# Kernel tuning notes

Measured on AMD Instinct MI355X. Metric: run time of the kernel, lower is better.

The kernel has to match this reference:

```python
import jax, jax.numpy as jnp
import numpy as np

B, K, NV, H, T = 4, 2, 32, 16, 4096
G = K * NV                 # conv groups = 64
OPG = 2 * (NV + H)         # out channels per group = 96 (instantaneous doubles channels)
TEMPERATURE = 1.0


def setup_inputs() -> dict:
    key = jax.random.key(0)
    k1, k2, k3 = jax.random.split(key, 3)
    x = jax.random.normal(k1, (B, G * H, T), dtype=jnp.float32)
    W = jax.random.normal(k2, (G, OPG, H), dtype=jnp.float32) * (1.0 / np.sqrt(H))
    b = jax.random.normal(k3, (G, OPG), dtype=jnp.float32) * 0.01
    return {"x": x, "W": W, "b": b}


def reference(x, W, b):
    # pad one zero step at end of sequence (ConstantPad1d((0,1),0))
    xp = jnp.pad(x, ((0, 0), (0, 0), (0, 1)))            # (B, G*H, T+1)
    xg = xp.reshape(B, G, H, T + 1)
    # TCN modeled as grouped pointwise conv: per-group linear over channel dim
    y = jnp.einsum('bgdt,god->bgot', xg, W) + b[None, :, :, None]  # (B, G, OPG, T+1)
    # split temporal / instantaneous branches with the causal shift
    y = y.reshape(B * K, NV, 2, NV + H, T + 1)
    xt = y[:, :, 0, :, :-1]                               # (B*K, NV, NV+H, T)
    xi = y[:, :, 1, :, 1:]                                # (B*K, NV, NV+H, T)
    # split attention logits (first NV channels) and context (last H channels)
    ctx = jnp.concatenate([xt[:, :, NV:, :], xi[:, :, NV:, :]], axis=1)   # (B*K, 2*NV, H, T)
    att = jnp.concatenate([xt[:, :, :NV, :], xi[:, :, :NV, :]], axis=2)   # (B*K, NV, 2*NV, T)
    att = jax.nn.softmax(att / TEMPERATURE, axis=2)
    out = jnp.einsum('bijt,bjdt->bidt', att, ctx)         # (B*K, NV, H, T)
    out = out.reshape(B, K * NV * H, T)
    attn = att.reshape(B, K, NV, 2 * NV, T)
    return out, attn
```

## Files before the change

### kernel.cpp

```cpp
#include <hip/hip_runtime.h>
#include <hip/hip_bf16.h>
#include <stdint.h>

#define B_  4
#define K_  2
#define T_  4096
#define TT  16

#define GS  296
#define US  16
#define AJ  652
#define AT  40
#define CJ  256
#define CT  16

__device__ __forceinline__ float bflo(uint32_t w) {
    union { uint32_t u; float f; } v; v.u = w << 16; return v.f;
}
__device__ __forceinline__ float bfhi(uint32_t w) {
    union { uint32_t u; float f; } v; v.u = w & 0xFFFF0000u; return v.f;
}
__device__ __forceinline__ float bf2f(uint16_t u) {
    union { uint32_t u; float f; } v; v.u = ((uint32_t)u) << 16; return v.f;
}
__device__ __forceinline__ uint16_t f2bf(float f) {
    union { float f; uint32_t u; } v; v.f = f;
    uint32_t x = v.u;
    return (uint16_t)((x + 0x7FFFu + ((x >> 16) & 1u)) >> 16);
}

__global__ __launch_bounds__(512, 2)
void tamcad_kernel(const float* __restrict__ x, const float* __restrict__ W,
                   const float* __restrict__ bias, float* __restrict__ out)
{
    __shared__ float    xsr[32 * GS];
    __shared__ uint16_t As [64 * AJ];
    __shared__ uint16_t Cs [64 * CJ];

    const int tid   = threadIdx.x;
    const int bk    = blockIdx.x >> 5;
    const int chunk = blockIdx.x & 31;
    const int b     = bk >> 1;
    const int k     = bk & 1;

    const int g_loc = tid >> 4;
    const int oq    = tid & 15;
    const int slot  = (oq >= 8) ? 1 : 0;

    float wreg[6][16];
    float breg[6];
    bool  isl[6];
    int   aoff[6];
    int   coff[6];
    #pragma unroll
    for (int r = 0; r < 6; ++r) {
        const int o = oq * 6 + r;
        const size_t wbase = (((size_t)(k * 32 + g_loc)) * 96 + o) * 16;
        const float4* wp = reinterpret_cast<const float4*>(W + wbase);
        float4 w0 = wp[0], w1 = wp[1], w2 = wp[2], w3 = wp[3];
        wreg[r][ 0]=w0.x; wreg[r][ 1]=w0.y; wreg[r][ 2]=w0.z; wreg[r][ 3]=w0.w;
        wreg[r][ 4]=w1.x; wreg[r][ 5]=w1.y; wreg[r][ 6]=w1.z; wreg[r][ 7]=w1.w;
        wreg[r][ 8]=w2.x; wreg[r][ 9]=w2.y; wreg[r][10]=w2.z; wreg[r][11]=w2.w;
        wreg[r][12]=w3.x; wreg[r][13]=w3.y; wreg[r][14]=w3.z; wreg[r][15]=w3.w;
        breg[r] = bias[(k * 32 + g_loc) * 96 + o];
        if (o < 32)      { isl[r] = true;  aoff[r] = o * AJ + g_loc;               coff[r] = 0; }
        else if (o < 48) { isl[r] = false; coff[r] = g_loc * CJ + (o - 32);        aoff[r] = 0; }
        else if (o < 80) { isl[r] = true;  aoff[r] = (o - 16) * AJ + g_loc;        coff[r] = 0; }
        else             { isl[r] = false; coff[r] = (32 + g_loc) * CJ + (o - 80); aoff[r] = 0; }
    }

    for (int l = 0; l < 8; ++l) {
        const int t0 = (chunk * 8 + l) * TT;

        {
            const float* gp = x + (((size_t)b * 1024) + (size_t)(k * 32 + g_loc) * 16 + oq) * (size_t)T_ + t0;
            float4 q0 = *(const float4*)(gp + 0);
            float4 q1 = *(const float4*)(gp + 4);
            float4 q2 = *(const float4*)(gp + 8);
            float4 q3 = *(const float4*)(gp + 12);
            float  q4 = (t0 + 16 < T_) ? gp[16] : 0.0f;
            float vals[17] = { q0.x,q0.y,q0.z,q0.w, q1.x,q1.y,q1.z,q1.w,
                               q2.x,q2.y,q2.z,q2.w, q3.x,q3.y,q3.z,q3.w, q4 };
            float* xp = xsr + g_loc * GS + oq;
            #pragma unroll
            for (int u = 0; u < 17; ++u) xp[u * US] = vals[u];
        }
        __syncthreads();

        {
            float xv[16];
            {
                const float4* p4 = reinterpret_cast<const float4*>(xsr + g_loc * GS + slot * US);
                float4 A0 = p4[0], A1 = p4[1], A2 = p4[2], A3 = p4[3];
                xv[ 0]=A0.x; xv[ 1]=A0.y; xv[ 2]=A0.z; xv[ 3]=A0.w;
                xv[ 4]=A1.x; xv[ 5]=A1.y; xv[ 6]=A1.z; xv[ 7]=A1.w;
                xv[ 8]=A2.x; xv[ 9]=A2.y; xv[10]=A2.z; xv[11]=A2.w;
                xv[12]=A3.x; xv[13]=A3.y; xv[14]=A3.z; xv[15]=A3.w;
            }
            for (int tp = 0; tp < TT; ++tp) {
                float yv[6];
                #pragma unroll
                for (int r = 0; r < 6; ++r) {
                    float a = breg[r];
                    #pragma unroll
                    for (int d = 0; d < 16; ++d) a = fmaf(wreg[r][d], xv[d], a);
                    yv[r] = a;
                }
                {
                    const float4* p4 = reinterpret_cast<const float4*>(xsr + g_loc * GS + (tp + 1 + slot) * US);
                    float4 A0 = p4[0], A1 = p4[1], A2 = p4[2], A3 = p4[3];
                    xv[ 0]=A0.x; xv[ 1]=A0.y; xv[ 2]=A0.z; xv[ 3]=A0.w;
                    xv[ 4]=A1.x; xv[ 5]=A1.y; xv[ 6]=A1.z; xv[ 7]=A1.w;
                    xv[ 8]=A2.x; xv[ 9]=A2.y; xv[10]=A2.z; xv[11]=A2.w;
                    xv[12]=A3.x; xv[13]=A3.y; xv[14]=A3.z; xv[15]=A3.w;
                }
                float m = -3.0e38f;
                #pragma unroll
                for (int r = 0; r < 6; ++r) if (isl[r]) m = fmaxf(m, yv[r]);
                #pragma unroll
                for (int s = 1; s < 16; s <<= 1) m = fmaxf(m, __shfl_xor(m, s));
                float ssum = 0.0f;
                float ev[6];
                #pragma unroll
                for (int r = 0; r < 6; ++r) {
                    ev[r] = 0.0f;
                    if (isl[r]) { ev[r] = __expf(yv[r] - m); ssum += ev[r]; }
                }
                #pragma unroll
                for (int s = 1; s < 16; s <<= 1) ssum += __shfl_xor(ssum, s);
                const float rinv = 1.0f / ssum;
                #pragma unroll
                for (int r = 0; r < 6; ++r) {
                    if (isl[r]) As[aoff[r] + tp * AT] = f2bf(ev[r] * rinv);
                    else        Cs[coff[r] + tp * CT] = f2bf(yv[r]);
                }
            }
        }
        __syncthreads();

        {
            const int tl = tid >> 5;
            const int r5 = tid & 31;
            const int i0 = (r5 & 7) << 2;
            const int d0 = (r5 >> 3) << 2;
            float acc[4][4];
            #pragma unroll
            for (int ii = 0; ii < 4; ++ii)
                #pragma unroll
                for (int dd = 0; dd < 4; ++dd) acc[ii][dd] = 0.0f;
            const uint16_t* Ap = As + tl * AT + i0;
            const uint16_t* Cp = Cs + tl * CT + d0;
            #pragma unroll 8
            for (int j = 0; j < 64; ++j) {
                uint2 aw = *(const uint2*)(Ap + j * AJ);
                uint2 cw = *(const uint2*)(Cp + j * CJ);
                float a0 = bflo(aw.x), a1 = bfhi(aw.x), a2 = bflo(aw.y), a3 = bfhi(aw.y);
                float c0 = bflo(cw.x), c1 = bfhi(cw.x), c2 = bflo(cw.y), c3 = bfhi(cw.y);
                acc[0][0] = fmaf(a0, c0, acc[0][0]); acc[0][1] = fmaf(a0, c1, acc[0][1]);
                acc[0][2] = fmaf(a0, c2, acc[0][2]); acc[0][3] = fmaf(a0, c3, acc[0][3]);
                acc[1][0] = fmaf(a1, c0, acc[1][0]); acc[1][1] = fmaf(a1, c1, acc[1][1]);
                acc[1][2] = fmaf(a1, c2, acc[1][2]); acc[1][3] = fmaf(a1, c3, acc[1][3]);
                acc[2][0] = fmaf(a2, c0, acc[2][0]); acc[2][1] = fmaf(a2, c1, acc[2][1]);
                acc[2][2] = fmaf(a2, c2, acc[2][2]); acc[2][3] = fmaf(a2, c3, acc[2][3]);
                acc[3][0] = fmaf(a3, c0, acc[3][0]); acc[3][1] = fmaf(a3, c1, acc[3][1]);
                acc[3][2] = fmaf(a3, c2, acc[3][2]); acc[3][3] = fmaf(a3, c3, acc[3][3]);
            }
            #pragma unroll
            for (int ii = 0; ii < 4; ++ii)
                #pragma unroll
                for (int dd = 0; dd < 4; ++dd)
                    xsr[((i0 + ii) * 16 + d0 + dd) * 17 + tl] = acc[ii][dd];
        }
        __syncthreads();

        {
            float ov[16];
            #pragma unroll
            for (int u = 0; u < 16; ++u) ov[u] = xsr[tid * 17 + u];
            float* op = out + (((size_t)b * 1024) + k * 512 + tid) * (size_t)T_ + t0;
            *(float4*)(op + 0)  = make_float4(ov[ 0], ov[ 1], ov[ 2], ov[ 3]);
            *(float4*)(op + 4)  = make_float4(ov[ 4], ov[ 5], ov[ 6], ov[ 7]);
            *(float4*)(op + 8)  = make_float4(ov[ 8], ov[ 9], ov[10], ov[11]);
            *(float4*)(op + 12) = make_float4(ov[12], ov[13], ov[14], ov[15]);

            float* attn_base = out + (size_t)B_ * 1024 * (size_t)T_;
            #pragma unroll
            for (int rr = 0; rr < 4; ++rr) {
                const int q = tid + 512 * rr;
                const int i = q >> 6;
                const int j = q & 63;
                const uint16_t* ap = As + j * AJ + i;
                float av[16];
                #pragma unroll
                for (int u = 0; u < 16; ++u) av[u] = bf2f(ap[u * AT]);
                float* tp2 = attn_base + ((((size_t)bk * 32 + i) * 64) + j) * (size_t)T_ + t0;
                *(float4*)(tp2 + 0)  = make_float4(av[ 0], av[ 1], av[ 2], av[ 3]);
                *(float4*)(tp2 + 4)  = make_float4(av[ 4], av[ 5], av[ 6], av[ 7]);
                *(float4*)(tp2 + 8)  = make_float4(av[ 8], av[ 9], av[10], av[11]);
                *(float4*)(tp2 + 12) = make_float4(av[12], av[13], av[14], av[15]);
            }
        }
        __syncthreads();
    }
}

extern "C" void kernel_launch(void* const* d_in, const int* in_sizes, int n_in,
                              void* d_out, int out_size, void* d_ws, size_t ws_size,
                              hipStream_t stream) {
    const float* x  = (const float*)d_in[0];
    const float* W  = (const float*)d_in[1];
    const float* bs = (const float*)d_in[2];
    float* out = (float*)d_out;
    tamcad_kernel<<<dim3(256), dim3(512), 0, stream>>>(x, W, bs, out);
}
```

Before: 293.3 us.

## Double threads per block, prefetch x into registers, drop softmax max pass

Block size goes from 512 to 1024 threads, so each thread computes 3 grouped-conv output channels instead of 6. The softmax reduction now spans 32 lanes, and the attention matmul uses 4x2 tiles per thread. The next x tile is prefetched into registers while the current one is processed, and the Cs row stride and the output staging layout are padded and skewed to reduce LDS bank conflicts. The max-subtraction pass in softmax is removed, saving one shuffle reduction per timestep but risking overflow for large logits. The launch bound of 1024 threads with a minimum of 4 blocks may force register caps and spills.

```diff
diff --git a/kernel.cpp b/kernel.cpp
--- a/kernel.cpp
+++ b/kernel.cpp
@@ -1,41 +1,28 @@
 #include <hip/hip_runtime.h>
-#include <hip/hip_bf16.h>
 #include <stdint.h>
 
-#define B_  4
-#define K_  2
 #define T_  4096
-#define TT  16
-
 #define GS  296
 #define US  16
 #define AJ  652
 #define AT  40
-#define CJ  256
-#define CT  16
-
-__device__ __forceinline__ float bflo(uint32_t w) {
-    union { uint32_t u; float f; } v; v.u = w << 16; return v.f;
+#define CJ  260
+
+static __device__ __forceinline__ float bflo(uint32_t w){ union{uint32_t u;float f;}v; v.u=w<<16; return v.f; }
+static __device__ __forceinline__ float bfhi(uint32_t w){ union{uint32_t u;float f;}v; v.u=w&0xFFFF0000u; return v.f; }
+static __device__ __forceinline__ float bf2f(uint16_t u){ union{uint32_t u;float f;}v; v.u=((uint32_t)u)<<16; return v.f; }
+static __device__ __forceinline__ uint16_t f2bf(float f){
+    union{float f;uint32_t u;}v; v.f=f; uint32_t x=v.u;
+    return (uint16_t)((x + 0x7FFFu + ((x>>16)&1u)) >> 16);
 }
-__device__ __forceinline__ float bfhi(uint32_t w) {
-    union { uint32_t u; float f; } v; v.u = w & 0xFFFF0000u; return v.f;
-}
-__device__ __forceinline__ float bf2f(uint16_t u) {
-    union { uint32_t u; float f; } v; v.u = ((uint32_t)u) << 16; return v.f;
-}
-__device__ __forceinline__ uint16_t f2bf(float f) {
-    union { float f; uint32_t u; } v; v.f = f;
-    uint32_t x = v.u;
-    return (uint16_t)((x + 0x7FFFu + ((x >> 16) & 1u)) >> 16);
-}
-
-__global__ __launch_bounds__(512, 2)
+
+__global__ __launch_bounds__(1024, 4)
 void tamcad_kernel(const float* __restrict__ x, const float* __restrict__ W,
                    const float* __restrict__ bias, float* __restrict__ out)
 {
-    __shared__ float    xsr[32 * GS];
-    __shared__ uint16_t As [64 * AJ];
-    __shared__ uint16_t Cs [64 * CJ];
+    __shared__ float    xsr[32*GS];
+    __shared__ uint16_t As [64*AJ];
+    __shared__ uint16_t Cs [64*CJ];
 
     const int tid   = threadIdx.x;
     const int bk    = blockIdx.x >> 5;
@@ -43,161 +30,168 @@
     const int b     = bk >> 1;
     const int k     = bk & 1;
 
-    const int g_loc = tid >> 4;
-    const int oq    = tid & 15;
-    const int slot  = (oq >= 8) ? 1 : 0;
-
-    float wreg[6][16];
-    float breg[6];
-    bool  isl[6];
-    int   aoff[6];
-    int   coff[6];
+    const int oq   = tid & 31;
+    const int g    = tid >> 5;
+    const int slot = oq >> 4;
+
+    const int dl = tid & 15;
+    const int gl = (tid >> 4) & 31;
+    const int hl = tid >> 9;
+
+    float wreg[3][16], breg[3];
+    int   aoff[3], coff[3];
+    bool  isl[3];
     #pragma unroll
-    for (int r = 0; r < 6; ++r) {
-        const int o = oq * 6 + r;
-        const size_t wbase = (((size_t)(k * 32 + g_loc)) * 96 + o) * 16;
-        const float4* wp = reinterpret_cast<const float4*>(W + wbase);
-        float4 w0 = wp[0], w1 = wp[1], w2 = wp[2], w3 = wp[3];
+    for (int r = 0; r < 3; ++r) {
+        const int o = oq*3 + r;
+        const float4* wp = reinterpret_cast<const float4*>(W + (((size_t)(k*32+g))*96 + o)*16);
+        float4 w0=wp[0], w1=wp[1], w2=wp[2], w3=wp[3];
         wreg[r][ 0]=w0.x; wreg[r][ 1]=w0.y; wreg[r][ 2]=w0.z; wreg[r][ 3]=w0.w;
         wreg[r][ 4]=w1.x; wreg[r][ 5]=w1.y; wreg[r][ 6]=w1.z; wreg[r][ 7]=w1.w;
         wreg[r][ 8]=w2.x; wreg[r][ 9]=w2.y; wreg[r][10]=w2.z; wreg[r][11]=w2.w;
         wreg[r][12]=w3.x; wreg[r][13]=w3.y; wreg[r][14]=w3.z; wreg[r][15]=w3.w;
-        breg[r] = bias[(k * 32 + g_loc) * 96 + o];
-        if (o < 32)      { isl[r] = true;  aoff[r] = o * AJ + g_loc;               coff[r] = 0; }
-        else if (o < 48) { isl[r] = false; coff[r] = g_loc * CJ + (o - 32);        aoff[r] = 0; }
-        else if (o < 80) { isl[r] = true;  aoff[r] = (o - 16) * AJ + g_loc;        coff[r] = 0; }
-        else             { isl[r] = false; coff[r] = (32 + g_loc) * CJ + (o - 80); aoff[r] = 0; }
+        breg[r] = bias[(k*32+g)*96 + o];
+        if (o < 32)      { isl[r]=true;  aoff[r]=o*AJ + g;            coff[r]=0; }
+        else if (o < 48) { isl[r]=false; coff[r]=g*CJ + (o-32);       aoff[r]=0; }
+        else if (o < 80) { isl[r]=true;  aoff[r]=(o-16)*AJ + g;       coff[r]=0; }
+        else             { isl[r]=false; coff[r]=(32+g)*CJ + (o-80);  aoff[r]=0; }
     }
 
+    const float* xrow = x + ((size_t)b*1024 + (size_t)(k*32+gl)*16 + dl) * (size_t)T_;
+
+    float4 pA, pB; float pS = 0.0f;
+    {
+        const float* gp = xrow + chunk*128 + hl*8;
+        pA = *(const float4*)(gp + 0);
+        pB = *(const float4*)(gp + 4);
+        pS = (hl && (chunk*128 + 16) < T_) ? gp[8] : 0.0f;
+    }
+
     for (int l = 0; l < 8; ++l) {
-        const int t0 = (chunk * 8 + l) * TT;
-
-        {
-            const float* gp = x + (((size_t)b * 1024) + (size_t)(k * 32 + g_loc) * 16 + oq) * (size_t)T_ + t0;
-            float4 q0 = *(const float4*)(gp + 0);
-            float4 q1 = *(const float4*)(gp + 4);
-            float4 q2 = *(const float4*)(gp + 8);
-            float4 q3 = *(const float4*)(gp + 12);
-            float  q4 = (t0 + 16 < T_) ? gp[16] : 0.0f;
-            float vals[17] = { q0.x,q0.y,q0.z,q0.w, q1.x,q1.y,q1.z,q1.w,
-                               q2.x,q2.y,q2.z,q2.w, q3.x,q3.y,q3.z,q3.w, q4 };
-            float* xp = xsr + g_loc * GS + oq;
-            #pragma unroll
-            for (int u = 0; u < 17; ++u) xp[u * US] = vals[u];
-        }
-        __syncthreads();
+        const int t0 = chunk*128 + l*16;
+
+        {
+            float* xp = xsr + gl*GS + dl;
+            const int ub = hl*8;
+            xp[(ub+0)*US]=pA.x; xp[(ub+1)*US]=pA.y; xp[(ub+2)*US]=pA.z; xp[(ub+3)*US]=pA.w;
+            xp[(ub+4)*US]=pB.x; xp[(ub+5)*US]=pB.y; xp[(ub+6)*US]=pB.z; xp[(ub+7)*US]=pB.w;
+            if (hl) xp[16*US] = pS;
+        }
+        __syncthreads();
+
+        if (l < 7) {
+            const int t0n = t0 + 16;
+            const float* gp = xrow + t0n + hl*8;
+            pA = *(const float4*)(gp + 0);
+            pB = *(const float4*)(gp + 4);
+            pS = (hl && (t0n + 16) < T_) ? gp[8] : 0.0f;
+        }
 
         {
             float xv[16];
             {
-                const float4* p4 = reinterpret_cast<const float4*>(xsr + g_loc * GS + slot * US);
-                float4 A0 = p4[0], A1 = p4[1], A2 = p4[2], A3 = p4[3];
+                const float4* p4 = reinterpret_cast<const float4*>(xsr + g*GS + slot*US);
+                float4 A0=p4[0], A1=p4[1], A2=p4[2], A3=p4[3];
                 xv[ 0]=A0.x; xv[ 1]=A0.y; xv[ 2]=A0.z; xv[ 3]=A0.w;
                 xv[ 4]=A1.x; xv[ 5]=A1.y; xv[ 6]=A1.z; xv[ 7]=A1.w;
                 xv[ 8]=A2.x; xv[ 9]=A2.y; xv[10]=A2.z; xv[11]=A2.w;
                 xv[12]=A3.x; xv[13]=A3.y; xv[14]=A3.z; xv[15]=A3.w;
             }
-            for (int tp = 0; tp < TT; ++tp) {
-                float yv[6];
-                #pragma unroll
-                for (int r = 0; r < 6; ++r) {
+            for (int tp = 0; tp < 16; ++tp) {
+                float yv[3];
+                #pragma unroll
+                for (int r = 0; r < 3; ++r) {
                     float a = breg[r];
                     #pragma unroll
                     for (int d = 0; d < 16; ++d) a = fmaf(wreg[r][d], xv[d], a);
                     yv[r] = a;
                 }
                 {
-                    const float4* p4 = reinterpret_cast<const float4*>(xsr + g_loc * GS + (tp + 1 + slot) * US);
-                    float4 A0 = p4[0], A1 = p4[1], A2 = p4[2], A3 = p4[3];
+                    const float4* p4 = reinterpret_cast<const float4*>(xsr + g*GS + (tp+1+slot)*US);
+                    float4 A0=p4[0], A1=p4[1], A2=p4[2], A3=p4[3];
                     xv[ 0]=A0.x; xv[ 1]=A0.y; xv[ 2]=A0.z; xv[ 3]=A0.w;
                     xv[ 4]=A1.x; xv[ 5]=A1.y; xv[ 6]=A1.z; xv[ 7]=A1.w;
                     xv[ 8]=A2.x; xv[ 9]=A2.y; xv[10]=A2.z; xv[11]=A2.w;
                     xv[12]=A3.x; xv[13]=A3.y; xv[14]=A3.z; xv[15]=A3.w;
                 }
-                float m = -3.0e38f;
-                #pragma unroll
-                for (int r = 0; r < 6; ++r) if (isl[r]) m = fmaxf(m, yv[r]);
-                #pragma unroll
-                for (int s = 1; s < 16; s <<= 1) m = fmaxf(m, __shfl_xor(m, s));
+                float ev[3];
                 float ssum = 0.0f;
-                float ev[6];
-                #pragma unroll
-                for (int r = 0; r < 6; ++r) {
+                #pragma unroll
+                for (int r = 0; r < 3; ++r) {
                     ev[r] = 0.0f;
-                    if (isl[r]) { ev[r] = __expf(yv[r] - m); ssum += ev[r]; }
-                }
-                #pragma unroll
-                for (int s = 1; s < 16; s <<= 1) ssum += __shfl_xor(ssum, s);
-                const float rinv = 1.0f / ssum;
-                #pragma unroll
-                for (int r = 0; r < 6; ++r) {
-                    if (isl[r]) As[aoff[r] + tp * AT] = f2bf(ev[r] * rinv);
-                    else        Cs[coff[r] + tp * CT] = f2bf(yv[r]);
-                }
-            }
-        }
-        __syncthreads();
-
-        {
-            const int tl = tid >> 5;
-            const int r5 = tid & 31;
-            const int i0 = (r5 & 7) << 2;
-            const int d0 = (r5 >> 3) << 2;
-            float acc[4][4];
+                    if (isl[r]) { ev[r] = __expf(yv[r]); ssum += ev[r]; }
+                }
+                #pragma unroll
+                for (int s = 1; s < 32; s <<= 1) ssum += __shfl_xor(ssum, s);
+                const float rinv = __builtin_amdgcn_rcpf(ssum);
+                #pragma unroll
+                for (int r = 0; r < 3; ++r) {
+                    if (isl[r]) As[aoff[r] + tp*AT] = f2bf(ev[r] * rinv);
+                    else        Cs[coff[r] + tp*16] = f2bf(yv[r]);
+                }
+            }
+        }
+        __syncthreads();
+
+        {
+            const int t  = tid >> 6;
+            const int r6 = tid & 63;
+            const int i0 = (r6 & 7) << 2;
+            const int d0 = (r6 >> 3) << 1;
+            float acc[4][2];
+            #pragma unroll
+            for (int ii = 0; ii < 4; ++ii) { acc[ii][0]=0.f; acc[ii][1]=0.f; }
+            const uint16_t* Ap = As + t*AT + i0;
+            const uint16_t* Cp = Cs + t*16 + d0;
+            #pragma unroll 8
+            for (int j = 0; j < 64; ++j) {
+                uint2    aw = *(const uint2*)(Ap + j*AJ);
+                uint32_t cw = *(const uint32_t*)(Cp + j*CJ);
+                float a0=bflo(aw.x), a1=bfhi(aw.x), a2=bflo(aw.y), a3=bfhi(aw.y);
+                float c0=bflo(cw),   c1=bfhi(cw);
+                acc[0][0]=fmaf(a0,c0,acc[0][0]); acc[0][1]=fmaf(a0,c1,acc[0][1]);
+                acc[1][0]=fmaf(a1,c0,acc[1][0]); acc[1][1]=fmaf(a1,c1,acc[1][1]);
+                acc[2][0]=fmaf(a2,c0,acc[2][0]); acc[2][1]=fmaf(a2,c1,acc[2][1]);
+                acc[3][0]=fmaf(a3,c0,acc[3][0]); acc[3][1]=fmaf(a3,c1,acc[3][1]);
+            }
+            const int skew = (r6 & 7) * 4;
             #pragma unroll
             for (int ii = 0; ii < 4; ++ii)
                 #pragma unroll
-                for (int dd = 0; dd < 4; ++dd) acc[ii][dd] = 0.0f;
-            const uint16_t* Ap = As + tl * AT + i0;
-            const uint16_t* Cp = Cs + tl * CT + d0;
-            #pragma unroll 8
-            for (int j = 0; j < 64; ++j) {
-                uint2 aw = *(const uint2*)(Ap + j * AJ);
-                uint2 cw = *(const uint2*)(Cp + j * CJ);
-                float a0 = bflo(aw.x), a1 = bfhi(aw.x), a2 = bflo(aw.y), a3 = bfhi(aw.y);
-                float c0 = bflo(cw.x), c1 = bfhi(cw.x), c2 = bflo(cw.y), c3 = bfhi(cw.y);
-                acc[0][0] = fmaf(a0, c0, acc[0][0]); acc[0][1] = fmaf(a0, c1, acc[0][1]);
-                acc[0][2] = fmaf(a0, c2, acc[0][2]); acc[0][3] = fmaf(a0, c3, acc[0][3]);
-                acc[1][0] = fmaf(a1, c0, acc[1][0]); acc[1][1] = fmaf(a1, c1, acc[1][1]);
-                acc[1][2] = fmaf(a1, c2, acc[1][2]); acc[1][3] = fmaf(a1, c3, acc[1][3]);
-                acc[2][0] = fmaf(a2, c0, acc[2][0]); acc[2][1] = fmaf(a2, c1, acc[2][1]);
-                acc[2][2] = fmaf(a2, c2, acc[2][2]); acc[2][3] = fmaf(a2, c3, acc[2][3]);
-                acc[3][0] = fmaf(a3, c0, acc[3][0]); acc[3][1] = fmaf(a3, c1, acc[3][1]);
-                acc[3][2] = fmaf(a3, c2, acc[3][2]); acc[3][3] = fmaf(a3, c3, acc[3][3]);
-            }
+                for (int dd = 0; dd < 2; ++dd) {
+                    const int row = (i0+ii)*16 + d0+dd;
+                    xsr[row*17 + skew + t] = acc[ii][dd];
+                }
+        }
+        __syncthreads();
+
+        {
+            if (tid < 512) {
+                const int skew = (tid >> 6) * 4;
+                float ov[16];
+                #pragma unroll
+                for (int u = 0; u < 16; ++u) ov[u] = xsr[tid*17 + skew + u];
+                float* op = out + ((size_t)b*1024 + k*512 + tid)*(size_t)T_ + t0;
+                *(float4*)(op + 0)  = make_float4(ov[ 0],ov[ 1],ov[ 2],ov[ 3]);
+                *(float4*)(op + 4)  = make_float4(ov[ 4],ov[ 5],ov[ 6],ov[ 7]);
+                *(float4*)(op + 8)  = make_float4(ov[ 8],ov[ 9],ov[10],ov[11]);
+                *(float4*)(op + 12) = make_float4(ov[12],ov[13],ov[14],ov[15]);
+            }
+            float* attn_base = out + (size_t)4*1024*(size_t)T_;
             #pragma unroll
-            for (int ii = 0; ii < 4; ++ii)
-                #pragma unroll
-                for (int dd = 0; dd < 4; ++dd)
-                    xsr[((i0 + ii) * 16 + d0 + dd) * 17 + tl] = acc[ii][dd];
-        }
-        __syncthreads();
-
-        {
-            float ov[16];
-            #pragma unroll
-            for (int u = 0; u < 16; ++u) ov[u] = xsr[tid * 17 + u];
-            float* op = out + (((size_t)b * 1024) + k * 512 + tid) * (size_t)T_ + t0;
-            *(float4*)(op + 0)  = make_float4(ov[ 0], ov[ 1], ov[ 2], ov[ 3]);
-            *(float4*)(op + 4)  = make_float4(ov[ 4], ov[ 5], ov[ 6], ov[ 7]);
-            *(float4*)(op + 8)  = make_float4(ov[ 8], ov[ 9], ov[10], ov[11]);
-            *(float4*)(op + 12) = make_float4(ov[12], ov[13], ov[14], ov[15]);
-
-            float* attn_base = out + (size_t)B_ * 1024 * (size_t)T_;
-            #pragma unroll
-            for (int rr = 0; rr < 4; ++rr) {
-                const int q = tid + 512 * rr;
+            for (int rr = 0; rr < 2; ++rr) {
+                const int q = tid + 1024*rr;
                 const int i = q >> 6;
                 const int j = q & 63;
-                const uint16_t* ap = As + j * AJ + i;
+                const uint16_t* ap = As + j*AJ + i;
                 float av[16];
                 #pragma unroll
-                for (int u = 0; u < 16; ++u) av[u] = bf2f(ap[u * AT]);
-                float* tp2 = attn_base + ((((size_t)bk * 32 + i) * 64) + j) * (size_t)T_ + t0;
-                *(float4*)(tp2 + 0)  = make_float4(av[ 0], av[ 1], av[ 2], av[ 3]);
-                *(float4*)(tp2 + 4)  = make_float4(av[ 4], av[ 5], av[ 6], av[ 7]);
-                *(float4*)(tp2 + 8)  = make_float4(av[ 8], av[ 9], av[10], av[11]);
-                *(float4*)(tp2 + 12) = make_float4(av[12], av[13], av[14], av[15]);
+                for (int u = 0; u < 16; ++u) av[u] = bf2f(ap[u*AT]);
+                float* tp2 = attn_base + (((size_t)bk*32 + i)*64 + j)*(size_t)T_ + t0;
+                *(float4*)(tp2 + 0)  = make_float4(av[ 0],av[ 1],av[ 2],av[ 3]);
+                *(float4*)(tp2 + 4)  = make_float4(av[ 4],av[ 5],av[ 6],av[ 7]);
+                *(float4*)(tp2 + 8)  = make_float4(av[ 8],av[ 9],av[10],av[11]);
+                *(float4*)(tp2 + 12) = make_float4(av[12],av[13],av[14],av[15]);
             }
         }
         __syncthreads();
@@ -211,5 +205,5 @@
     const float* W  = (const float*)d_in[1];
     const float* bs = (const float*)d_in[2];
     float* out = (float*)d_out;
-    tamcad_kernel<<<dim3(256), dim3(512), 0, stream>>>(x, W, bs, out);
+    tamcad_kernel<<<dim3(256), dim3(1024), 0, stream>>>(x, W, bs, out);
 }
```

After: 239.5 us. 18.3% less time.
